# Kernel tuning notes

Measured on AMD Instinct MI355X. Metric: run time of the kernel, lower is better.

The kernel has to match this reference:

```python
import jax, jax.numpy as jnp
import numpy as np

EPS = 1e-5
C, FR, T = 256, 7, 251  # channel, frequency, time
B = 32


def _bn(x, p, axis):
    # p: stacked [gamma, beta, running_mean, running_var] (eval-mode BatchNorm)
    g, b, m, v = p
    scale = g * jax.lax.rsqrt(v + EPS)
    shape = [1] * x.ndim
    shape[axis] = -1
    return x * scale.reshape(shape) + (b - m * scale).reshape(shape)


def _branch(xr, qw, qbn, kw, kbn, lbn):
    # xr: [N, Cin, L]. conv1x1 (no bias) + BN1d over channel axis.
    q = _bn(jnp.einsum('oc,ncl->nol', qw, xr), qbn, 1)
    k = _bn(jnp.einsum('oc,ncl->nol', kw, xr), kbn, 1)
    # adaptive_avg_pool2d((1, L)) on [N,1,Cin,L]: mean over channel axis, identity on L
    qv = q.mean(axis=1)  # [N, L]
    kv = k.mean(axis=1)  # [N, L]
    logits = qv[:, :, None] * kv[:, None, :]  # outer product == matmul(q^T, k): [N, L, L]
    g, b, m, v = lbn[:, 0]  # BatchNorm2d(1), eval mode -> scalar affine
    scale = g * jax.lax.rsqrt(v + EPS)
    w = jax.nn.softmax(logits * scale + (b - m * scale), axis=-1)
    # einsum 'bhxy,ihh->bhxy' == v * sum_i diag(w_i); return the diagonal sum [L]
    return jnp.einsum('nii->i', w)


def setup_inputs() -> dict:
    key = jax.random.key(0)
    ks = jax.random.split(key, 20)

    def w(k, o, i):
        return jax.random.normal(k, (o, i), jnp.float32) * 0.05

    def bn(k, n):
        k1, k2, k3, k4 = jax.random.split(k, 4)
        gamma = 1.0 + 0.1 * jax.random.normal(k1, (n,), jnp.float32)
        beta = 0.1 * jax.random.normal(k2, (n,), jnp.float32)
        mean = 0.1 * jax.random.normal(k3, (n,), jnp.float32)
        var = jnp.abs(1.0 + 0.1 * jax.random.normal(k4, (n,), jnp.float32))
        return jnp.stack([gamma, beta, mean, var])

    return {
        'x': jax.random.normal(ks[0], (B, C, FR, T), jnp.float32),
        'qc_w': w(ks[1], T, T), 'qc_bn': bn(ks[2], T),
        'kc_w': w(ks[3], T, T), 'kc_bn': bn(ks[4], T),
        'lc_bn': bn(ks[5], 1),
        'qf_w': w(ks[6], C, C), 'qf_bn': bn(ks[7], C),
        'kf_w': w(ks[8], C, C), 'kf_bn': bn(ks[9], C),
        'lf_bn': bn(ks[10], 1),
        'qt_w': w(ks[11], C, C), 'qt_bn': bn(ks[12], C),
        'kt_w': w(ks[13], C, C), 'kt_bn': bn(ks[14], C),
        'lt_bn': bn(ks[15], 1),
        'v_w': w(ks[16], C, C),
        'v_b': 0.05 * jax.random.normal(ks[17], (C,), jnp.float32),
        'v_bn': bn(ks[18], C),
    }


def reference(x, qc_w, qc_bn, kc_w, kc_bn, lc_bn,
              qf_w, qf_bn, kf_w, kf_bn, lf_bn,
              qt_w, qt_bn, kt_w, kt_bn, lt_bn,
              v_w, v_b, v_bn):
    b = x.shape[0]
    # x: [B, C, FR, T]
    x_c = x.transpose(0, 2, 3, 1).reshape(b * FR, T, C)   # conv over T channels
    x_f = x.transpose(0, 2, 1, 3).reshape(b * FR, C, T)   # conv over C channels
    x_t = x.transpose(0, 3, 1, 2).reshape(b * T, C, FR)   # conv over C channels
    dc = _branch(x_c, qc_w, qc_bn, kc_w, kc_bn, lc_bn)    # [C] (attention over channel axis of v)
    df = _branch(x_f, qf_w, qf_bn, kf_w, kf_bn, lf_bn)    # [T]
    dt = _branch(x_t, qt_w, qt_bn, kt_w, kt_bn, lt_bn)    # [FR]
    v = _bn(jnp.einsum('oc,bcxy->boxy', v_w, x) + v_b[None, :, None, None], v_bn, 1)
    # v_c + v_f + v_t + x, where each v_* = v scaled by summed attention diagonal
    return v * (dc[None, :, None, None] + dt[None, None, :, None] + df[None, None, None, :]) + x
```

## Files before the change

kernel.cpp:

```cpp
#include <hip/hip_runtime.h>

typedef unsigned short u16;
typedef __attribute__((ext_vector_type(8))) short short8;
typedef __attribute__((ext_vector_type(4))) float float4v;
typedef __attribute__((ext_vector_type(4))) int int4v;
typedef __attribute__((ext_vector_type(2))) int int2v;

#define EPS 1e-5f
#define NC 256
#define NT 251
#define NF 7
#define NSP 1757
#define NB 32

#define OFF_QEC 0
#define OFF_KEC 256
#define OFF_QEF 512
#define OFF_KEF 768
#define OFF_QET 1024
#define OFF_KET 1280
#define OFF_VSC 1536
#define OFF_VOF 1792
#define OFF_CONST 2048
#define OFF_DC 2064
#define OFF_DF 2320
#define OFF_DT 2576
#define WS_END 2592
#define OFF_QT 2592
#define OFF_KT (OFF_QT+56320)
#define WS2_END (OFF_KT+56320)
#define OFF_WB16 WS2_END
#define WS3_END (WS2_END+32768)
#define OFF_QF2 WS3_END
#define OFF_KF2 (OFF_QF2+56320)
#define OFF_QCS (OFF_KF2+56320)
#define OFF_KCS (OFF_QCS+57344)
#define WS4_END (OFF_KCS+57344)

#define XSW(kg, w) ((kg)*256 + ((w) ^ ((((kg)>>1)&3)<<3)))

__device__ __forceinline__ u16 f2b(float f) {
    unsigned int u = __float_as_uint(f);
    return (u16)((u + 0x7FFFu + ((u >> 16) & 1u)) >> 16);
}

__global__ __launch_bounds__(256) void prep_kernel(
    const float* qc_w, const float* qc_bn, const float* kc_w, const float* kc_bn, const float* lc_bn,
    const float* qf_w, const float* qf_bn, const float* kf_w, const float* kf_bn, const float* lf_bn,
    const float* qt_w, const float* qt_bn, const float* kt_w, const float* kt_bn, const float* lt_bn,
    const float* v_b, const float* v_bn, const float* v_w, float* ws)
{
    int tid = threadIdx.x;
    int blk = blockIdx.x;
    __shared__ float sc[256];
    __shared__ float red[256];
    if (blk < 24) {
        int m = blk >> 2, j = blk & 3;
        const float* w; const float* bn; float* out; int O;
        switch (m) {
            case 0: w=qc_w; bn=qc_bn; out=ws+OFF_QEC; O=NT; break;
            case 1: w=kc_w; bn=kc_bn; out=ws+OFF_KEC; O=NT; break;
            case 2: w=qf_w; bn=qf_bn; out=ws+OFF_QEF; O=NC; break;
            case 3: w=kf_w; bn=kf_bn; out=ws+OFF_KEF; O=NC; break;
            case 4: w=qt_w; bn=qt_bn; out=ws+OFF_QET; O=NC; break;
            default: w=kt_w; bn=kt_bn; out=ws+OFF_KET; O=NC; break;
        }
        if (tid < O) sc[tid] = bn[tid] * rsqrtf(bn[3*O+tid] + EPS);
        __syncthreads();
        int tl = tid & 63, kc4 = tid >> 6;
        int t = j*64 + tl;
        float acc = 0.f;
        if (t < O) {
            #pragma unroll 8
            for (int o = kc4; o < O; o += 4)
                acc = fmaf(sc[o], w[(size_t)o*O + t], acc);
        }
        red[tid] = acc;
        __syncthreads();
        if (tid < 64) {
            int tt = j*64 + tid;
            if (tt < O)
                out[tt] = (red[tid] + red[tid+64] + red[tid+128] + red[tid+192]) / (float)O;
        }
        if (j == 0) {
            float bs = 0.f;
            if (tid < O) bs = bn[O+tid] - bn[2*O+tid]*sc[tid];
            __syncthreads();
            red[tid] = bs; __syncthreads();
            for (int s2 = 128; s2 > 0; s2 >>= 1) { if (tid < s2) red[tid] += red[tid+s2]; __syncthreads(); }
            if (tid == 0) ws[OFF_CONST+m] = red[0] / (float)O;
        }
    } else if (blk == 24) {
        if (tid < NC) {
            float s = v_bn[tid] * rsqrtf(v_bn[3*NC+tid] + EPS);
            ws[OFF_VSC+tid] = s;
            ws[OFF_VOF+tid] = v_bn[NC+tid] - v_bn[2*NC+tid]*s + v_b[tid]*s;
        }
        if (tid == 0) {
            ws[OFF_CONST+6] = lc_bn[0] * rsqrtf(lc_bn[3] + EPS);
            ws[OFF_CONST+7] = lf_bn[0] * rsqrtf(lf_bn[3] + EPS);
            ws[OFF_CONST+8] = lt_bn[0] * rsqrtf(lt_bn[3] + EPS);
        }
        for (int i = tid; i < WS_END - OFF_DC; i += 256) ws[OFF_DC + i] = 0.f;
    } else {
        u16* wb = (u16*)(ws + OFF_WB16);
        int base = (blk - 25) * 8192;
        for (int i4 = tid; i4 < 2048; i4 += 256) {
            int e = base + i4*4;
            int o = e >> 8, k = e & 255;
            float4v v = *(const float4v*)(v_w + e);
            u16 h0 = f2b(v.x), h1 = f2b(v.y), h2 = f2b(v.z), h3 = f2b(v.w);
            int r = ((o>>7)<<3) | (k>>5);
            int q = (((o>>4)&7)<<9) | (((k>>3)&3)<<7) | ((o&15)<<3) | (k&7);
            unsigned long long pk = (unsigned long long)h0 | ((unsigned long long)h1<<16)
                                  | ((unsigned long long)h2<<32) | ((unsigned long long)h3<<48);
            *(unsigned long long*)&wb[(r<<12) | q] = pk;
        }
    }
}

__global__ __launch_bounds__(512) void qv_kernel(const float* __restrict__ x,
                                                 float* __restrict__ ws)
{
    __shared__ float lds[8608];
    int tid = threadIdx.x;
    int blk = blockIdx.x;
    const float* cst = ws + OFF_CONST;

    if (blk < 1792) {
        int n = blk >> 3, cb = blk & 7;
        int b = n / NF, f = n % NF;
        const float* xb = x + (size_t)b*NC*NSP + (size_t)f*NT + (size_t)(cb*32)*NSP;
        if (tid < NT) lds[8096+tid] = ws[OFF_QEC+tid];
        else if (tid >= 256 && tid < 256+NT) lds[8352+tid-256] = ws[OFF_KEC+tid-256];
        int lr = tid >> 8, lane = tid & 255;
        #pragma unroll 4
        for (int i = 0; i < 16; ++i) {
            int r = 2*i + lr;
            if (lane < NT) lds[r*253 + lane] = xb[(size_t)r*NSP + lane];
        }
        __syncthreads();
        int r = tid >> 4, q = tid & 15;
        float qa = 0.f, ka = 0.f;
        #pragma unroll
        for (int i = 0; i < 16; ++i) {
            int t = q + 16*i;
            if (t < NT) {
                float xv = lds[r*253 + t];
                qa = fmaf(lds[8096+t], xv, qa);
                ka = fmaf(lds[8352+t], xv, ka);
            }
        }
        qa += __shfl_xor(qa, 1);  ka += __shfl_xor(ka, 1);
        qa += __shfl_xor(qa, 2);  ka += __shfl_xor(ka, 2);
        qa += __shfl_xor(qa, 4);  ka += __shfl_xor(ka, 4);
        qa += __shfl_xor(qa, 8);  ka += __shfl_xor(ka, 8);
        if (q == 0) {
            int ch = cb*32 + r;
            ws[OFF_QCS + n*256 + ch] = qa;
            ws[OFF_KCS + n*256 + ch] = ka;
        }
    } else {
        int fb = blk - 1792;
        int b = fb / 14, nchunk = fb % 14;
        int n0 = nchunk * 128;
        int spg = tid & 31, chg = tid >> 5;
        if (tid < 256) { lds[5120+tid] = ws[OFF_QEF+tid]; lds[5632+tid] = ws[OFF_QET+tid]; }
        else { int u = tid-256; lds[5376+u] = ws[OFF_KEF+u]; lds[5888+u] = ws[OFF_KET+u]; }
        __syncthreads();
        const size_t xbase = (size_t)b*NC*NSP;
        int sp0 = n0 + spg*4;
        bool full = (sp0 + 3 < NSP);
        float qf[4]={0,0,0,0}, kf[4]={0,0,0,0}, qt[4]={0,0,0,0}, kt[4]={0,0,0,0};
        #pragma unroll 4
        for (int i = 0; i < 16; ++i) {
            int ch = chg*16 + i;
            const float* xr = x + xbase + (size_t)ch*NSP + sp0;
            float xv[4];
            if (full) {
                xv[0]=xr[0]; xv[1]=xr[1]; xv[2]=xr[2]; xv[3]=xr[3];
            } else {
                #pragma unroll
                for (int j = 0; j < 4; ++j) xv[j] = (sp0+j < NSP) ? xr[j] : 0.f;
            }
            float eqf = lds[5120+ch], ekf = lds[5376+ch];
            float eqt = lds[5632+ch], ekt = lds[5888+ch];
            #pragma unroll
            for (int j = 0; j < 4; ++j) {
                qf[j] = fmaf(eqf, xv[j], qf[j]);
                kf[j] = fmaf(ekf, xv[j], kf[j]);
                qt[j] = fmaf(eqt, xv[j], qt[j]);
                kt[j] = fmaf(ekt, xv[j], kt[j]);
            }
        }
        #pragma unroll
        for (int j = 0; j < 4; ++j) {
            qf[j] += __shfl_xor(qf[j], 32);
            kf[j] += __shfl_xor(kf[j], 32);
            qt[j] += __shfl_xor(qt[j], 32);
            kt[j] += __shfl_xor(kt[j], 32);
        }
        int wv = tid >> 6, ln = tid & 63;
        if (ln < 32) {
            int base = wv*640 + ln*20;
            #pragma unroll
            for (int j = 0; j < 4; ++j) {
                lds[base+j]    = qf[j];
                lds[base+4+j]  = kf[j];
                lds[base+8+j]  = qt[j];
                lds[base+12+j] = kt[j];
            }
        }
        __syncthreads();
        if (tid < 32) {
            float acc[16];
            #pragma unroll
            for (int j = 0; j < 16; ++j) acc[j] = 0.f;
            #pragma unroll
            for (int w = 0; w < 8; ++w) {
                int base = w*640 + tid*20;
                #pragma unroll
                for (int j = 0; j < 16; ++j) acc[j] += lds[base+j];
            }
            int sp0w = n0 + tid*4;
            #pragma unroll
            for (int j = 0; j < 4; ++j) {
                if (sp0w + j < NSP) {
                    size_t o = (size_t)b*1760 + sp0w + j;
                    ws[OFF_QF2 + o] = acc[j]    + cst[2];
                    ws[OFF_KF2 + o] = acc[4+j]  + cst[3];
                    ws[OFF_QT  + o] = acc[8+j]  + cst[4];
                    ws[OFF_KT  + o] = acc[12+j] + cst[5];
                }
            }
        }
    }
}

__global__ __launch_bounds__(256) void sm_kernel(float* __restrict__ ws)
{
    __shared__ float kv[NC];
    __shared__ float kv2[NT];
    __shared__ float dt_acc[NF];
    int tid = threadIdx.x, blk = blockIdx.x;
    const float* cst = ws + OFF_CONST;

    if (blk < 224) {
        int b = blk / NF, f = blk % NF;
        float qcv = ws[OFF_QCS + blk*256 + tid] + cst[0];
        float kcv = ws[OFF_KCS + blk*256 + tid] + cst[1];
        kv[tid] = kcv;
        float qfv = 0.f, kfv = 0.f;
        if (tid < NT) {
            size_t o = (size_t)b*1760 + f*NT + tid;
            qfv = ws[OFF_QF2 + o];
            kfv = ws[OFF_KF2 + o];
            kv2[tid] = kfv;
        }
        __syncthreads();
        {
            float s = cst[6];
            float qi = s * qcv;
            float m0=-1e30f, m1=-1e30f, m2=-1e30f, m3=-1e30f;
            #pragma unroll 2
            for (int jj = 0; jj < NC; jj += 4) {
                m0 = fmaxf(m0, qi*kv[jj]);
                m1 = fmaxf(m1, qi*kv[jj+1]);
                m2 = fmaxf(m2, qi*kv[jj+2]);
                m3 = fmaxf(m3, qi*kv[jj+3]);
            }
            float m = fmaxf(fmaxf(m0,m1), fmaxf(m2,m3));
            float d0=0.f, d1=0.f, d2=0.f, d3=0.f;
            #pragma unroll 2
            for (int jj = 0; jj < NC; jj += 4) {
                d0 += __expf(qi*kv[jj]   - m);
                d1 += __expf(qi*kv[jj+1] - m);
                d2 += __expf(qi*kv[jj+2] - m);
                d3 += __expf(qi*kv[jj+3] - m);
            }
            float den = (d0+d1)+(d2+d3);
            atomicAdd(&ws[OFF_DC + tid], __expf(qi*kcv - m)/den);
        }
        if (tid < NT) {
            float s = cst[7];
            float qi = s * qfv;
            float m0=-1e30f, m1=-1e30f, m2=-1e30f, m3=-1e30f;
            int jj = 0;
            #pragma unroll 2
            for (; jj + 3 < NT; jj += 4) {
                m0 = fmaxf(m0, qi*kv2[jj]);
                m1 = fmaxf(m1, qi*kv2[jj+1]);
                m2 = fmaxf(m2, qi*kv2[jj+2]);
                m3 = fmaxf(m3, qi*kv2[jj+3]);
            }
            for (; jj < NT; ++jj) m0 = fmaxf(m0, qi*kv2[jj]);
            float m = fmaxf(fmaxf(m0,m1), fmaxf(m2,m3));
            float d0=0.f, d1=0.f, d2=0.f, d3=0.f;
            jj = 0;
            #pragma unroll 2
            for (; jj + 3 < NT; jj += 4) {
                d0 += __expf(qi*kv2[jj]   - m);
                d1 += __expf(qi*kv2[jj+1] - m);
                d2 += __expf(qi*kv2[jj+2] - m);
                d3 += __expf(qi*kv2[jj+3] - m);
            }
            for (; jj < NT; ++jj) d0 += __expf(qi*kv2[jj] - m);
            float den = (d0+d1)+(d2+d3);
            atomicAdd(&ws[OFF_DF + tid], __expf(qi*kfv - m)/den);
        }
    } else {
        int b = blk - 224;
        if (tid < NF) dt_acc[tid] = 0.f;
        __syncthreads();
        if (tid < NT) {
            float s = cst[8];
            float q[NF], k[NF];
            #pragma unroll
            for (int i = 0; i < NF; ++i) {
                size_t o = (size_t)b*1760 + i*NT + tid;
                q[i] = ws[OFF_QT + o];
                k[i] = ws[OFF_KT + o];
            }
            #pragma unroll
            for (int i = 0; i < NF; ++i) {
                float qi = s * q[i];
                float m = -1e30f;
                #pragma unroll
                for (int j = 0; j < NF; ++j) m = fmaxf(m, qi*k[j]);
                float den = 0.f;
                #pragma unroll
                for (int j = 0; j < NF; ++j) den += __expf(qi*k[j] - m);
                atomicAdd(&dt_acc[i], __expf(qi*k[i] - m)/den);
            }
        }
        __syncthreads();
        if (tid < NF) atomicAdd(&ws[OFF_DT + tid], dt_acc[tid]);
    }
}

__global__ __launch_bounds__(512) void qkt_kernel(const float* __restrict__ x,
                                                  float* __restrict__ ws, int fuse_t)
{
    __shared__ float kv[NC];
    __shared__ float p0[512], p1[512], p2[512], p3[512];
    int tid = threadIdx.x;
    int bid = blockIdx.x;
    int n = bid >> 1, role = bid & 1;
    int b = n / NF, f = n % NF;
    const float* xb = x + (size_t)b*NC*NSP + (size_t)f*NT;
    const float* cst = ws + OFF_CONST;
    int half = tid >> 8, lid = tid & 255;

    if (role == 0) {
        const float* xrow = xb + (size_t)lid*NSP;
        const float* qeC = ws + OFF_QEC;  const float* keC = ws + OFF_KEC;
        float qc = 0.f, kc = 0.f;
        int t0 = half ? 126 : 0, t1 = half ? NT : 126;
        #pragma unroll 16
        for (int t = t0; t < t1; ++t) {
            float xv = xrow[t];
            qc = fmaf(qeC[t], xv, qc);
            kc = fmaf(keC[t], xv, kc);
        }
        p0[tid] = qc; p1[tid] = kc;
        __syncthreads();
        if (tid < 256) {
            qc = p0[tid] + p0[tid+256] + cst[0];
            kc = p1[tid] + p1[tid+256] + cst[1];
            kv[tid] = kc;
        }
        __syncthreads();
        if (tid < 256) {
            float s = cst[6];
            float qi = s * qc;
            float m0=-1e30f, m1=-1e30f, m2=-1e30f, m3=-1e30f;
            #pragma unroll 2
            for (int jj = 0; jj < NC; jj += 4) {
                m0 = fmaxf(m0, qi*kv[jj]);
                m1 = fmaxf(m1, qi*kv[jj+1]);
                m2 = fmaxf(m2, qi*kv[jj+2]);
                m3 = fmaxf(m3, qi*kv[jj+3]);
            }
            float m = fmaxf(fmaxf(m0,m1), fmaxf(m2,m3));
            float d0=0.f, d1=0.f, d2=0.f, d3=0.f;
            #pragma unroll 2
            for (int jj = 0; jj < NC; jj += 4) {
                d0 += __expf(qi*kv[jj]   - m);
                d1 += __expf(qi*kv[jj+1] - m);
                d2 += __expf(qi*kv[jj+2] - m);
                d3 += __expf(qi*kv[jj+3] - m);
            }
            float den = (d0+d1)+(d2+d3);
            atomicAdd(&ws[OFF_DC + tid], __expf(qi*kv[tid] - m)/den);
        }
    } else {
        float qf=0.f, kf=0.f, qt=0.f, kt=0.f;
        if (lid < NT) {
            const float* xc = xb + lid + (size_t)(half*128)*NSP;
            const float* qeF = ws + OFF_QEF + half*128;  const float* keF = ws + OFF_KEF + half*128;
            const float* qeT = ws + OFF_QET + half*128;  const float* keT = ws + OFF_KET + half*128;
            #pragma unroll 8
            for (int ch = 0; ch < 128; ++ch) {
                float xv = xc[(size_t)ch*NSP];
                qf = fmaf(qeF[ch], xv, qf);
                kf = fmaf(keF[ch], xv, kf);
                qt = fmaf(qeT[ch], xv, qt);
                kt = fmaf(keT[ch], xv, kt);
            }
        }
        p0[tid]=qf; p1[tid]=kf; p2[tid]=qt; p3[tid]=kt;
        __syncthreads();
        float qfv=0.f, kfv=0.f;
        if (tid < NT) {
            qfv = p0[tid] + p0[tid+256] + cst[2];
            kfv = p1[tid] + p1[tid+256] + cst[3];
            float qtv = p2[tid] + p2[tid+256] + cst[4];
            float ktv = p3[tid] + p3[tid+256] + cst[5];
            kv[tid] = kfv;
            if (fuse_t) {
                ws[OFF_QT + ((size_t)b*NT + tid)*NF + f] = qtv;
                ws[OFF_KT + ((size_t)b*NT + tid)*NF + f] = ktv;
            }
        }
        __syncthreads();
        if (tid < NT) {
            float s = cst[7];
            float qi = s * qfv;
            float m0=-1e30f, m1=-1e30f, m2=-1e30f, m3=-1e30f;
            int jj = 0;
            #pragma unroll 2
            for (; jj + 3 < NT; jj += 4) {
                m0 = fmaxf(m0, qi*kv[jj]);
                m1 = fmaxf(m1, qi*kv[jj+1]);
                m2 = fmaxf(m2, qi*kv[jj+2]);
                m3 = fmaxf(m3, qi*kv[jj+3]);
            }
            for (; jj < NT; ++jj) m0 = fmaxf(m0, qi*kv[jj]);
            float m = fmaxf(fmaxf(m0,m1), fmaxf(m2,m3));
            float d0=0.f, d1=0.f, d2=0.f, d3=0.f;
            jj = 0;
            #pragma unroll 2
            for (; jj + 3 < NT; jj += 4) {
                d0 += __expf(qi*kv[jj]   - m);
                d1 += __expf(qi*kv[jj+1] - m);
                d2 += __expf(qi*kv[jj+2] - m);
                d3 += __expf(qi*kv[jj+3] - m);
            }
            for (; jj < NT; ++jj) d0 += __expf(qi*kv[jj] - m);
            float den = (d0+d1)+(d2+d3);
            atomicAdd(&ws[OFF_DF + tid], __expf(qi*kfv - m)/den);
        }
    }
}

__global__ __launch_bounds__(256) void tsm_kernel(float* __restrict__ ws)
{
    __shared__ float dt_acc[NF];
    int tid = threadIdx.x, b = blockIdx.x;
    if (tid < NF) dt_acc[tid] = 0.f;
    __syncthreads();
    if (tid < NT) {
        float s = ws[OFF_CONST+8];
        const float* qp = ws + OFF_QT + ((size_t)b*NT + tid)*NF;
        const float* kp = ws + OFF_KT + ((size_t)b*NT + tid)*NF;
        float q[NF], k[NF];
        #pragma unroll
        for (int i = 0; i < NF; ++i) { q[i] = qp[i]; k[i] = kp[i]; }
        #pragma unroll
        for (int i = 0; i < NF; ++i) {
            float qi = s * q[i];
            float m = -1e30f;
            #pragma unroll
            for (int j = 0; j < NF; ++j) m = fmaxf(m, qi*k[j]);
            float den = 0.f;
            #pragma unroll
            for (int j = 0; j < NF; ++j) den += __expf(qi*k[j] - m);
            atomicAdd(&dt_acc[i], __expf(qi*k[i] - m)/den);
        }
    }
    __syncthreads();
    if (tid < NF) atomicAdd(&ws[OFF_DT + tid], dt_acc[tid]);
}

__global__ __launch_bounds__(256) void t_kernel(const float* __restrict__ x, float* __restrict__ ws)
{
    __shared__ float qs[32*NF], ks[32*NF], dt_acc[NF];
    int tid = threadIdx.x;
    int b  = blockIdx.x >> 3;
    int t0 = (blockIdx.x & 7) * 32;
    int tl = tid & 31, fr = tid >> 5;
    int t = t0 + tl;
    bool act = (fr < NF) && (t < NT);
    if (tid < NF) dt_acc[tid] = 0.f;

    float aq = 0.f, ak = 0.f;
    const float* qeT = ws + OFF_QET;
    const float* keT = ws + OFF_KET;
    if (act) {
        const float* xr = x + (size_t)b*NC*NSP + fr*NT + t;
        #pragma unroll 8
        for (int ch = 0; ch < NC; ++ch) {
            float xv = xr[(size_t)ch*NSP];
            aq = fmaf(qeT[ch], xv, aq);
            ak = fmaf(keT[ch], xv, ak);
        }
    }
    __syncthreads();
    if (act) {
        qs[tl*NF + fr] = aq + ws[OFF_CONST+4];
        ks[tl*NF + fr] = ak + ws[OFF_CONST+5];
    }
    __syncthreads();
    if (act) {
        float s = ws[OFF_CONST+8];
        float qi = s * qs[tl*NF + fr];
        float m = -1e30f;
        #pragma unroll
        for (int j = 0; j < NF; ++j) m = fmaxf(m, qi*ks[tl*NF + j]);
        float den = 0.f;
        #pragma unroll
        for (int j = 0; j < NF; ++j) den += __expf(qi*ks[tl*NF + j] - m);
        atomicAdd(&dt_acc[fr], __expf(qi*ks[tl*NF + fr] - m)/den);
    }
    __syncthreads();
    if (tid < NF) atomicAdd(&ws[OFF_DT + tid], dt_acc[tid]);
}

template<int WBF>
__global__ __launch_bounds__(256) void main_kernel(
    const float* __restrict__ x, const float* __restrict__ vw,
    const float* __restrict__ ws, float* __restrict__ out)
{
    __shared__ u16 Ws[2][4096];
    __shared__ unsigned int Xs[2][2048];
    __shared__ float vsL[128], voL[128], dcL[128], dtfL[128];

    int tid = threadIdx.x;
    int flat = blockIdx.x;
    int xcd = flat & 7, idx = flat >> 3;
    int pair = xcd*56 + (idx >> 1);
    int o0 = (idx & 1) * 128;
    int n0 = (pair % 14) * 128;
    int b  = pair / 14;
    const size_t xbase = (size_t)b * NC * NSP;

    if (tid < 128) {
        int o = o0 + tid;
        vsL[tid] = ws[OFF_VSC+o];
        voL[tid] = ws[OFF_VOF+o];
        dcL[tid] = ws[OFF_DC+o];
        int nn = n0 + tid; if (nn > NSP-1) nn = NSP-1;
        int ff = nn / NT, tt = nn - ff*NT;
        dtfL[tid] = ws[OFF_DT+ff] + ws[OFF_DF+tt];
    }

    int wv = tid >> 6, ln = tid & 63;
    int quad = ln >> 4, l16 = ln & 15;
    int wr = wv >> 1, wc = wv & 1;

    float4v acc[4][4] = {};

    int kgs = tid >> 5, nbs = tid & 31;
    int oo = tid >> 1, half = tid & 1;

    const u16* wbg = nullptr;
    if constexpr (WBF) wbg = (const u16*)(ws + OFF_WB16) + (size_t)(o0 >> 7) * 32768;

    int4v wA, wB;
    float wf[16];
    float xv[4][4];

    auto loadW = [&](int ks) {
        if constexpr (WBF) {
            const int4v* wsrc = (const int4v*)(wbg + (size_t)ks*4096);
            wA = wsrc[tid]; wB = wsrc[256 + tid];
        } else {
            const float* wr4 = vw + (size_t)(o0+oo)*NC + ks*32 + half*16;
            #pragma unroll
            for (int c = 0; c < 16; ++c) wf[c] = wr4[c];
        }
    };
    auto loadX = [&](int ks) {
        int nbase = n0 + nbs*4;
        const float* xr = x + xbase + (size_t)(ks*32 + kgs*4)*NSP + nbase;
        if (nbase + 3 < NSP) {
            #pragma unroll
            for (int rr = 0; rr < 4; ++rr)
                #pragma unroll
                for (int i = 0; i < 4; ++i)
                    xv[rr][i] = xr[(size_t)rr*NSP + i];
        } else {
            #pragma unroll
            for (int rr = 0; rr < 4; ++rr)
                #pragma unroll
                for (int i = 0; i < 4; ++i)
                    xv[rr][i] = (nbase + i < NSP) ? xr[(size_t)rr*NSP + i] : 0.f;
        }
    };
    auto storeWX = [&](int bufi) {
        if constexpr (WBF) {
            *(int4v*)&Ws[bufi][tid*8]        = wA;
            *(int4v*)&Ws[bufi][2048 + tid*8] = wB;
        } else {
            union { u16 us[16]; short8 v[2]; } wb;
            #pragma unroll
            for (int c = 0; c < 16; ++c) wb.us[c] = f2b(wf[c]);
            int frg = oo >> 4, o16 = oo & 15;
            #pragma unroll
            for (int qq = 0; qq < 2; ++qq) {
                int qd = 2*half + qq;
                *(short8*)&Ws[bufi][frg*512 + qd*128 + o16*8] = wb.v[qq];
            }
        }
        unsigned int pk[8];
        #pragma unroll
        for (int i = 0; i < 4; ++i)
            #pragma unroll
            for (int jp = 0; jp < 2; ++jp)
                pk[i*2+jp] = (unsigned int)f2b(xv[2*jp][i])
                           | ((unsigned int)f2b(xv[2*jp+1][i]) << 16);
        *(int4v*)&Xs[bufi][XSW(kgs, nbs*8)]     = *(int4v*)&pk[0];
        *(int4v*)&Xs[bufi][XSW(kgs, nbs*8 + 4)] = *(int4v*)&pk[4];
    };

    loadW(0); loadX(0);
    storeWX(0);
    __syncthreads();

    for (int ks = 0; ks < 8; ++ks) {
        int cur = ks & 1;
        if (ks < 7) { loadW(ks+1); loadX(ks+1); }

        short8 afr[4], bfr[4];
        #pragma unroll
        for (int fr = 0; fr < 4; ++fr)
            afr[fr] = *(short8*)&Ws[cur][(wr*4+fr)*512 + ln*8];
        #pragma unroll
        for (int fc = 0; fc < 4; ++fc) {
            int nn = wc*64 + fc*16 + l16;
            int2v lo = *(int2v*)&Xs[cur][XSW(2*quad,   2*nn)];
            int2v hi = *(int2v*)&Xs[cur][XSW(2*quad+1, 2*nn)];
            union { int i4[4]; short8 v; } u;
            u.i4[0] = lo.x; u.i4[1] = lo.y; u.i4[2] = hi.x; u.i4[3] = hi.y;
            bfr[fc] = u.v;
        }
        #pragma unroll
        for (int fr = 0; fr < 4; ++fr)
            #pragma unroll
            for (int fc = 0; fc < 4; ++fc)
                acc[fr][fc] = __builtin_amdgcn_mfma_f32_16x16x32_bf16(
                    afr[fr], bfr[fc], acc[fr][fc], 0, 0, 0);

        if (ks < 7) storeWX(cur ^ 1);
        __syncthreads();
    }

    #pragma unroll
    for (int fr = 0; fr < 4; ++fr) {
        #pragma unroll
        for (int r = 0; r < 4; ++r) {
            int ol = wr*64 + fr*16 + quad*4 + r;
            int o = o0 + ol;
            float vs = vsL[ol], vo = voL[ol], dcv = dcL[ol];
            const size_t orow = xbase + (size_t)o*NSP;
            #pragma unroll
            for (int fc = 0; fc < 4; ++fc) {
                int nl = wc*64 + fc*16 + l16;
                int nn = n0 + nl;
                if (nn < NSP) {
                    size_t gi = orow + nn;
                    out[gi] = (acc[fr][fc][r]*vs + vo)*(dcv + dtfL[nl]) + x[gi];
                }
            }
        }
    }
}

extern "C" void kernel_launch(void* const* d_in, const int* in_sizes, int n_in,
                              void* d_out, int out_size, void* d_ws, size_t ws_size,
                              hipStream_t stream)
{
    const float* x    = (const float*)d_in[0];
    const float* qc_w = (const float*)d_in[1];  const float* qc_bn = (const float*)d_in[2];
    const float* kc_w = (const float*)d_in[3];  const float* kc_bn = (const float*)d_in[4];
    const float* lc_bn= (const float*)d_in[5];
    const float* qf_w = (const float*)d_in[6];  const float* qf_bn = (const float*)d_in[7];
    const float* kf_w = (const float*)d_in[8];  const float* kf_bn = (const float*)d_in[9];
    const float* lf_bn= (const float*)d_in[10];
    const float* qt_w = (const float*)d_in[11]; const float* qt_bn = (const float*)d_in[12];
    const float* kt_w = (const float*)d_in[13]; const float* kt_bn = (const float*)d_in[14];
    const float* lt_bn= (const float*)d_in[15];
    const float* v_w  = (const float*)d_in[16]; const float* v_b   = (const float*)d_in[17];
    const float* v_bn = (const float*)d_in[18];
    float* ws = (float*)d_ws;
    float* out = (float*)d_out;

    int fuse_t = (ws_size >= (size_t)WS2_END * sizeof(float)) ? 1 : 0;
    int wbf    = (ws_size >= (size_t)WS3_END * sizeof(float)) ? 1 : 0;
    int newq   = (ws_size >= (size_t)WS4_END * sizeof(float)) ? 1 : 0;

    prep_kernel<<<wbf ? 33 : 25, 256, 0, stream>>>(qc_w,qc_bn,kc_w,kc_bn,lc_bn,
                                                   qf_w,qf_bn,kf_w,kf_bn,lf_bn,
                                                   qt_w,qt_bn,kt_w,kt_bn,lt_bn,
                                                   v_b,v_bn,v_w,ws);
    if (newq) {
        qv_kernel<<<2240, 512, 0, stream>>>(x, ws);
        sm_kernel<<<256, 256, 0, stream>>>(ws);
    } else {
        qkt_kernel<<<NB*NF*2, 512, 0, stream>>>(x, ws, fuse_t);
        if (fuse_t) tsm_kernel<<<NB, 256, 0, stream>>>(ws);
        else        t_kernel<<<NB*8, 256, 0, stream>>>(x, ws);
    }
    if (wbf) main_kernel<1><<<896, 256, 0, stream>>>(x, v_w, ws, out);
    else     main_kernel<0><<<896, 256, 0, stream>>>(x, v_w, ws, out);
}
```

Baseline: 220.2 us.

## Pack x to bf16 MFMA layout in qv_kernel and add LDS-free main2 GEMM

The qv_kernel f/t pass already reads all of x, so it now also writes a bf16 copy of x, pre-swizzled into the MFMA fragment layout, into a workspace region. A new main2_kernel reads the pre-packed weight and x images straight from global memory into registers and skips the per-block LDS staging, conversion and barriers of the old main_kernel. The cost of converting x is moved out of the GEMM kernel. In exchange qv_kernel writes about 29 MB of extra data, main2 issues uncached fragment reads with no double buffering, and the path needs a much larger workspace, so it only runs if ws_size allows.

Result: slower. 224.7 us (+2.0%).

```diff
diff --git a/kernel.cpp b/kernel.cpp
--- a/kernel.cpp
+++ b/kernel.cpp
@@ -36,12 +36,18 @@
 #define OFF_QCS (OFF_KF2+56320)
 #define OFF_KCS (OFF_QCS+57344)
 #define WS4_END (OFF_KCS+57344)
+#define OFF_XB16 WS4_END
+#define XB16_U32 (448*16384)
+#define WS5_END (OFF_XB16 + XB16_U32)
 
 #define XSW(kg, w) ((kg)*256 + ((w) ^ ((((kg)>>1)&3)<<3)))
 
 __device__ __forceinline__ u16 f2b(float f) {
     unsigned int u = __float_as_uint(f);
     return (u16)((u + 0x7FFFu + ((u >> 16) & 1u)) >> 16);
+}
+__device__ __forceinline__ unsigned int pk2(float a, float b) {
+    return (unsigned int)f2b(a) | ((unsigned int)f2b(b) << 16);
 }
 
 __global__ __launch_bounds__(256) void prep_kernel(
@@ -120,7 +126,7 @@
 }
 
 __global__ __launch_bounds__(512) void qv_kernel(const float* __restrict__ x,
-                                                 float* __restrict__ ws)
+                                                 float* __restrict__ ws, int pack)
 {
     __shared__ float lds[8608];
     int tid = threadIdx.x;
@@ -171,26 +177,46 @@
         const size_t xbase = (size_t)b*NC*NSP;
         int sp0 = n0 + spg*4;
         bool full = (sp0 + 3 < NSP);
+        unsigned int* ximg = nullptr;
+        if (pack) ximg = (unsigned int*)(ws + OFF_XB16) + (size_t)(b*14 + nchunk)*16384;
+
         float qf[4]={0,0,0,0}, kf[4]={0,0,0,0}, qt[4]={0,0,0,0}, kt[4]={0,0,0,0};
-        #pragma unroll 4
-        for (int i = 0; i < 16; ++i) {
-            int ch = chg*16 + i;
-            const float* xr = x + xbase + (size_t)ch*NSP + sp0;
-            float xv[4];
-            if (full) {
-                xv[0]=xr[0]; xv[1]=xr[1]; xv[2]=xr[2]; xv[3]=xr[3];
-            } else {
+        #pragma unroll
+        for (int ii = 0; ii < 4; ++ii) {
+            int ch0 = chg*16 + ii*4;
+            float xv4[4][4];
+            #pragma unroll
+            for (int cc = 0; cc < 4; ++cc) {
+                int ch = ch0 + cc;
+                const float* xr = x + xbase + (size_t)ch*NSP + sp0;
+                if (full) {
+                    xv4[cc][0]=xr[0]; xv4[cc][1]=xr[1]; xv4[cc][2]=xr[2]; xv4[cc][3]=xr[3];
+                } else {
+                    #pragma unroll
+                    for (int j = 0; j < 4; ++j) xv4[cc][j] = (sp0+j < NSP) ? xr[j] : 0.f;
+                }
+                float eqf = lds[5120+ch], ekf = lds[5376+ch];
+                float eqt = lds[5632+ch], ekt = lds[5888+ch];
                 #pragma unroll
-                for (int j = 0; j < 4; ++j) xv[j] = (sp0+j < NSP) ? xr[j] : 0.f;
-            }
-            float eqf = lds[5120+ch], ekf = lds[5376+ch];
-            float eqt = lds[5632+ch], ekt = lds[5888+ch];
-            #pragma unroll
-            for (int j = 0; j < 4; ++j) {
-                qf[j] = fmaf(eqf, xv[j], qf[j]);
-                kf[j] = fmaf(ekf, xv[j], kf[j]);
-                qt[j] = fmaf(eqt, xv[j], qt[j]);
-                kt[j] = fmaf(ekt, xv[j], kt[j]);
+                for (int j = 0; j < 4; ++j) {
+                    qf[j] = fmaf(eqf, xv4[cc][j], qf[j]);
+                    kf[j] = fmaf(ekf, xv4[cc][j], kf[j]);
+                    qt[j] = fmaf(eqt, xv4[cc][j], qt[j]);
+                    kt[j] = fmaf(ekt, xv4[cc][j], kt[j]);
+                }
+            }
+            if (pack) {
+                int kgsg = ch0 >> 2;
+                int ks = kgsg >> 3, kgl = kgsg & 7;
+                unsigned int* dst = ximg + ks*2048 + kgl*256 + spg*8;
+                unsigned int pk[8];
+                #pragma unroll
+                for (int i = 0; i < 4; ++i) {
+                    pk[i*2+0] = pk2(xv4[0][i], xv4[1][i]);
+                    pk[i*2+1] = pk2(xv4[2][i], xv4[3][i]);
+                }
+                *(int4v*)&dst[0] = *(int4v*)&pk[0];
+                *(int4v*)&dst[4] = *(int4v*)&pk[4];
             }
         }
         #pragma unroll
@@ -526,6 +552,84 @@
     if (tid < NF) atomicAdd(&ws[OFF_DT + tid], dt_acc[tid]);
 }
 
+__global__ __launch_bounds__(256, 3) void main2_kernel(
+    const float* __restrict__ x, const float* __restrict__ ws, float* __restrict__ out)
+{
+    __shared__ float vsL[128], voL[128], dcL[128], dtfL[128];
+    int tid = threadIdx.x;
+    int flat = blockIdx.x;
+    int xcd = flat & 7, idx = flat >> 3;
+    int pair = xcd*56 + (idx >> 1);
+    int o0 = (idx & 1) * 128;
+    int n0 = (pair % 14) * 128;
+    int b  = pair / 14;
+    const size_t xbase = (size_t)b * NC * NSP;
+
+    if (tid < 128) {
+        int o = o0 + tid;
+        vsL[tid] = ws[OFF_VSC+o];
+        voL[tid] = ws[OFF_VOF+o];
+        dcL[tid] = ws[OFF_DC+o];
+        int nn = n0 + tid; if (nn > NSP-1) nn = NSP-1;
+        int ff = nn / NT, tt = nn - ff*NT;
+        dtfL[tid] = ws[OFF_DT+ff] + ws[OFF_DF+tt];
+    }
+    __syncthreads();
+
+    int wv = tid >> 6, ln = tid & 63;
+    int quad = ln >> 4, l16 = ln & 15;
+    int wr = wv >> 1, wc = wv & 1;
+
+    const u16* wimg = (const u16*)(ws + OFF_WB16) + (size_t)(o0 >> 7) * 32768;
+    const unsigned int* ximg = (const unsigned int*)(ws + OFF_XB16)
+                             + (size_t)(b*14 + (n0 >> 7)) * 16384;
+
+    float4v acc[4][4] = {};
+
+    #pragma unroll 2
+    for (int ks = 0; ks < 8; ++ks) {
+        short8 afr[4], bfr[4];
+        #pragma unroll
+        for (int fr = 0; fr < 4; ++fr)
+            afr[fr] = *(const short8*)&wimg[ks*4096 + (wr*4+fr)*512 + ln*8];
+        #pragma unroll
+        for (int fc = 0; fc < 4; ++fc) {
+            int nn = wc*64 + fc*16 + l16;
+            int2v lo = *(const int2v*)&ximg[ks*2048 + (2*quad)*256 + 2*nn];
+            int2v hi = *(const int2v*)&ximg[ks*2048 + (2*quad+1)*256 + 2*nn];
+            union { int i4[4]; short8 v; } u;
+            u.i4[0] = lo.x; u.i4[1] = lo.y; u.i4[2] = hi.x; u.i4[3] = hi.y;
+            bfr[fc] = u.v;
+        }
+        #pragma unroll
+        for (int fr = 0; fr < 4; ++fr)
+            #pragma unroll
+            for (int fc = 0; fc < 4; ++fc)
+                acc[fr][fc] = __builtin_amdgcn_mfma_f32_16x16x32_bf16(
+                    afr[fr], bfr[fc], acc[fr][fc], 0, 0, 0);
+    }
+
+    #pragma unroll
+    for (int fr = 0; fr < 4; ++fr) {
+        #pragma unroll
+        for (int r = 0; r < 4; ++r) {
+            int ol = wr*64 + fr*16 + quad*4 + r;
+            int o = o0 + ol;
+            float vs = vsL[ol], vo = voL[ol], dcv = dcL[ol];
+            const size_t orow = xbase + (size_t)o*NSP;
+            #pragma unroll
+            for (int fc = 0; fc < 4; ++fc) {
+                int nl = wc*64 + fc*16 + l16;
+                int nn = n0 + nl;
+                if (nn < NSP) {
+                    size_t gi = orow + nn;
+                    out[gi] = (acc[fr][fc][r]*vs + vo)*(dcv + dtfL[nl]) + x[gi];
+                }
+            }
+        }
+    }
+}
+
 template<int WBF>
 __global__ __launch_bounds__(256) void main_kernel(
     const float* __restrict__ x, const float* __restrict__ vw,
@@ -617,8 +721,7 @@
         for (int i = 0; i < 4; ++i)
             #pragma unroll
             for (int jp = 0; jp < 2; ++jp)
-                pk[i*2+jp] = (unsigned int)f2b(xv[2*jp][i])
-                           | ((unsigned int)f2b(xv[2*jp+1][i]) << 16);
+                pk[i*2+jp] = pk2(xv[2*jp][i], xv[2*jp+1][i]);
         *(int4v*)&Xs[bufi][XSW(kgs, nbs*8)]     = *(int4v*)&pk[0];
         *(int4v*)&Xs[bufi][XSW(kgs, nbs*8 + 4)] = *(int4v*)&pk[4];
     };
@@ -698,19 +801,24 @@
     int fuse_t = (ws_size >= (size_t)WS2_END * sizeof(float)) ? 1 : 0;
     int wbf    = (ws_size >= (size_t)WS3_END * sizeof(float)) ? 1 : 0;
     int newq   = (ws_size >= (size_t)WS4_END * sizeof(float)) ? 1 : 0;
+    int xb     = (ws_size >= (size_t)WS5_END * sizeof(float)) ? 1 : 0;
 
     prep_kernel<<<wbf ? 33 : 25, 256, 0, stream>>>(qc_w,qc_bn,kc_w,kc_bn,lc_bn,
                                                    qf_w,qf_bn,kf_w,kf_bn,lf_bn,
                                                    qt_w,qt_bn,kt_w,kt_bn,lt_bn,
                                                    v_b,v_bn,v_w,ws);
     if (newq) {
-        qv_kernel<<<2240, 512, 0, stream>>>(x, ws);
+        qv_kernel<<<2240, 512, 0, stream>>>(x, ws, xb);
         sm_kernel<<<256, 256, 0, stream>>>(ws);
     } else {
         qkt_kernel<<<NB*NF*2, 512, 0, stream>>>(x, ws, fuse_t);
         if (fuse_t) tsm_kernel<<<NB, 256, 0, stream>>>(ws);
         else        t_kernel<<<NB*8, 256, 0, stream>>>(x, ws);
     }
-    if (wbf) main_kernel<1><<<896, 256, 0, stream>>>(x, v_w, ws, out);
-    else     main_kernel<0><<<896, 256, 0, stream>>>(x, v_w, ws, out);
-}
+    if (xb && wbf)
+        main2_kernel<<<896, 256, 0, stream>>>(x, ws, out);
+    else if (wbf)
+        main_kernel<1><<<896, 256, 0, stream>>>(x, v_w, ws, out);
+    else
+        main_kernel<0><<<896, 256, 0, stream>>>(x, v_w, ws, out);
+}
```
